# Optimization experiments

Measured on AMD Instinct MI355X. Metric: run time of the kernel, lower is better.

The kernel has to match this reference:

```python
import jax, jax.numpy as jnp
import numpy as np

# Model constants (solved parameter set; precip and water_efficiency from source)
TS = 0.0001
PRECIP = 1.845
WATER_EFFICIENCY = 0.449
SEEP_RATE = 0.2
UPTAKE_RATE = 1.0
ETA = 3.0
Q = 1.0
MORT_RATE = 0.3
D2 = 1.0
D3 = 0.05


def laplacian(x):
    # 3x3 5-point Laplacian stencil with replicate (edge) padding, x: [B,1,H,W]
    xp = jnp.pad(x, ((0, 0), (0, 0), (1, 1), (1, 1)), mode='edge')
    return (xp[:, :, :-2, 1:-1] + xp[:, :, 2:, 1:-1]
            + xp[:, :, 1:-1, :-2] + xp[:, :, 1:-1, 2:] - 4.0 * x)


def setup_inputs() -> dict:
    key = jax.random.key(0)
    k1, k2, k3 = jax.random.split(key, 3)
    shape = (16, 1, 1024, 1024)
    w = jax.random.uniform(k1, shape, dtype=jnp.float32)
    b = jax.random.uniform(k2, shape, dtype=jnp.float32)
    T = jax.random.uniform(k3, shape, dtype=jnp.float32)
    return {"w": w, "b": b, "T": T}


def reference(w, b, T):
    uptake = UPTAKE_RATE * w * b * (1.0 + ETA * b ** Q)
    dw = (D2 * laplacian(w) - SEEP_RATE * w + PRECIP - uptake) * TS
    db = (D3 * laplacian(b) - MORT_RATE * T * b + WATER_EFFICIENCY * uptake) * TS
    return (w + dw, b + db)
```

## Files before the change

### kernel.cpp

```cpp
#include <hip/hip_runtime.h>


namespace {
constexpr int IMGS = 16;
constexpr int H = 1024;
constexpr int W = 1024;
constexpr size_t PLANE = (size_t)H * W;
}

__global__ __launch_bounds__(256) void nca_step(
    const float* __restrict__ wg, const float* __restrict__ bg,
    const float* __restrict__ Tg, float* __restrict__ owg,
    float* __restrict__ obg)
{
    const int nwg = gridDim.x;
    const int cpx = nwg >> 3;
    const int bid = blockIdx.x;
    const int swz = (bid & 7) * cpx + (bid >> 3);

    const int img = swz >> 10;
    const int y   = swz & (H - 1);
    const int t   = threadIdx.x;
    const int x0  = t << 2;

    const float* wp = wg + (size_t)img * PLANE;
    const float* bp = bg + (size_t)img * PLANE;
    const float* Tp = Tg + (size_t)img * PLANE;

    const int yu = (y > 0)     ? (y - 1) : 0;
    const int yd = (y < H - 1) ? (y + 1) : (H - 1);

    const float* wrow = wp + (size_t)y * W;
    const float* brow = bp + (size_t)y * W;

    const float4 cw = *(const float4*)(wrow + x0);
    const float4 uw = *(const float4*)(wp + (size_t)yu * W + x0);
    const float4 dw = *(const float4*)(wp + (size_t)yd * W + x0);
    const float4 cb = *(const float4*)(brow + x0);
    const float4 ub = *(const float4*)(bp + (size_t)yu * W + x0);
    const float4 db = *(const float4*)(bp + (size_t)yd * W + x0);
    const float4 cT = *(const float4*)(Tp + (size_t)y * W + x0);

    const float wl = (x0 > 0)     ? wrow[x0 - 1] : cw.x;
    const float wr = (x0 + 4 < W) ? wrow[x0 + 4] : cw.w;
    const float bl = (x0 > 0)     ? brow[x0 - 1] : cb.x;
    const float br = (x0 + 4 < W) ? brow[x0 + 4] : cb.w;

    float lw[4], lb[4];
    lw[0] = uw.x + dw.x + wl   + cw.y - 4.0f * cw.x;
    lw[1] = uw.y + dw.y + cw.x + cw.z - 4.0f * cw.y;
    lw[2] = uw.z + dw.z + cw.y + cw.w - 4.0f * cw.z;
    lw[3] = uw.w + dw.w + cw.z + wr   - 4.0f * cw.w;

    lb[0] = ub.x + db.x + bl   + cb.y - 4.0f * cb.x;
    lb[1] = ub.y + db.y + cb.x + cb.z - 4.0f * cb.y;
    lb[2] = ub.z + db.z + cb.y + cb.w - 4.0f * cb.z;
    lb[3] = ub.w + db.w + cb.z + br   - 4.0f * cb.w;

    const float wv[4] = {cw.x, cw.y, cw.z, cw.w};
    const float bv[4] = {cb.x, cb.y, cb.z, cb.w};
    const float Tv[4] = {cT.x, cT.y, cT.z, cT.w};

    float4 ow4, ob4;
    float* owp = &ow4.x;
    float* obp = &ob4.x;
#pragma unroll
    for (int i = 0; i < 4; ++i) {
        const float up = wv[i] * bv[i] * (1.0f + 3.0f * bv[i]);
        owp[i] = wv[i] + (lw[i] - 0.2f * wv[i] + 1.845f - up) * 1e-4f;
        obp[i] = bv[i] + (0.05f * lb[i] - 0.3f * Tv[i] * bv[i] + 0.449f * up) * 1e-4f;
    }

    const size_t oidx = (size_t)img * PLANE + (size_t)y * W + x0;
    *(float4*)(owg + oidx) = ow4;
    *(float4*)(obg + oidx) = ob4;
}

extern "C" void kernel_launch(void* const* d_in, const int* in_sizes, int n_in,
                              void* d_out, int out_size, void* d_ws, size_t ws_size,
                              hipStream_t stream) {
    const float* w = (const float*)d_in[0];
    const float* b = (const float*)d_in[1];
    const float* T = (const float*)d_in[2];
    float* ow = (float*)d_out;
    float* ob = ow + (size_t)IMGS * PLANE;

    dim3 grid(IMGS * H);
    dim3 block(W / 4);
    nca_step<<<grid, block, 0, stream>>>(w, b, T, ow, ob);
}
```

Baseline: 280.3 us.

## Process four rows per block with register row reuse, shuffles, nontemporal IO

Each block now computes four consecutive rows and keeps six rows of w and b in registers, so vertical neighbours are reused instead of reloaded. Horizontal neighbours come from wave shuffles, and only the edge lanes fall back to scalar global loads. T loads and the output stores use nontemporal hints to reduce cache pollution. The grid shrinks by a factor of four, and each thread holds more registers and more loads in flight.

```diff
diff --git a/kernel.cpp b/kernel.cpp
--- a/kernel.cpp
+++ b/kernel.cpp
@@ -6,7 +6,10 @@
 constexpr int H = 1024;
 constexpr int W = 1024;
 constexpr size_t PLANE = (size_t)H * W;
+constexpr int RPB = 4;
 }
+
+typedef float f4 __attribute__((ext_vector_type(4)));
 
 __global__ __launch_bounds__(256) void nca_step(
     const float* __restrict__ wg, const float* __restrict__ bg,
@@ -18,62 +21,75 @@
     const int bid = blockIdx.x;
     const int swz = (bid & 7) * cpx + (bid >> 3);
 
-    const int img = swz >> 10;
-    const int y   = swz & (H - 1);
-    const int t   = threadIdx.x;
-    const int x0  = t << 2;
+    const int img = swz >> 8;
+    const int r0  = (swz & 255) * RPB;
+    const int t    = threadIdx.x;
+    const int lane = t & 63;
+    const int x0   = t << 2;
 
     const float* wp = wg + (size_t)img * PLANE;
     const float* bp = bg + (size_t)img * PLANE;
     const float* Tp = Tg + (size_t)img * PLANE;
 
-    const int yu = (y > 0)     ? (y - 1) : 0;
-    const int yd = (y < H - 1) ? (y + 1) : (H - 1);
+    const int rm1 = (r0 > 0)       ? r0 - 1   : 0;
+    const int rp4 = (r0 + RPB < H) ? r0 + RPB : H - 1;
 
-    const float* wrow = wp + (size_t)y * W;
-    const float* brow = bp + (size_t)y * W;
+    f4 wv[RPB + 2], bv[RPB + 2], Tv[RPB];
+    wv[0] = *(const f4*)(wp + (size_t)rm1 * W + x0);
+    bv[0] = *(const f4*)(bp + (size_t)rm1 * W + x0);
+#pragma unroll
+    for (int i = 0; i < RPB; ++i) {
+        wv[i + 1] = *(const f4*)(wp + (size_t)(r0 + i) * W + x0);
+        bv[i + 1] = *(const f4*)(bp + (size_t)(r0 + i) * W + x0);
+        Tv[i] = __builtin_nontemporal_load((const f4*)(Tp + (size_t)(r0 + i) * W + x0));
+    }
+    wv[RPB + 1] = *(const f4*)(wp + (size_t)rp4 * W + x0);
+    bv[RPB + 1] = *(const f4*)(bp + (size_t)rp4 * W + x0);
 
-    const float4 cw = *(const float4*)(wrow + x0);
-    const float4 uw = *(const float4*)(wp + (size_t)yu * W + x0);
-    const float4 dw = *(const float4*)(wp + (size_t)yd * W + x0);
-    const float4 cb = *(const float4*)(brow + x0);
-    const float4 ub = *(const float4*)(bp + (size_t)yu * W + x0);
-    const float4 db = *(const float4*)(bp + (size_t)yd * W + x0);
-    const float4 cT = *(const float4*)(Tp + (size_t)y * W + x0);
+#pragma unroll
+    for (int i = 0; i < RPB; ++i) {
+        const f4 cw = wv[i + 1], uw = wv[i], dw = wv[i + 2];
+        const f4 cb = bv[i + 1], ub = bv[i], db = bv[i + 2];
+        const f4 cT = Tv[i];
 
-    const float wl = (x0 > 0)     ? wrow[x0 - 1] : cw.x;
-    const float wr = (x0 + 4 < W) ? wrow[x0 + 4] : cw.w;
-    const float bl = (x0 > 0)     ? brow[x0 - 1] : cb.x;
-    const float br = (x0 + 4 < W) ? brow[x0 + 4] : cb.w;
+        float wl = __shfl_up(cw.w, 1);
+        float wr = __shfl_down(cw.x, 1);
+        float bl = __shfl_up(cb.w, 1);
+        float br = __shfl_down(cb.x, 1);
+        const float* wrow = wp + (size_t)(r0 + i) * W;
+        const float* brow = bp + (size_t)(r0 + i) * W;
+        if (lane == 0) {
+            wl = (x0 > 0) ? wrow[x0 - 1] : cw.x;
+            bl = (x0 > 0) ? brow[x0 - 1] : cb.x;
+        }
+        if (lane == 63) {
+            wr = (x0 + 4 < W) ? wrow[x0 + 4] : cw.w;
+            br = (x0 + 4 < W) ? brow[x0 + 4] : cb.w;
+        }
 
-    float lw[4], lb[4];
-    lw[0] = uw.x + dw.x + wl   + cw.y - 4.0f * cw.x;
-    lw[1] = uw.y + dw.y + cw.x + cw.z - 4.0f * cw.y;
-    lw[2] = uw.z + dw.z + cw.y + cw.w - 4.0f * cw.z;
-    lw[3] = uw.w + dw.w + cw.z + wr   - 4.0f * cw.w;
+        f4 lw, lb;
+        lw.x = uw.x + dw.x + wl   + cw.y - 4.0f * cw.x;
+        lw.y = uw.y + dw.y + cw.x + cw.z - 4.0f * cw.y;
+        lw.z = uw.z + dw.z + cw.y + cw.w - 4.0f * cw.z;
+        lw.w = uw.w + dw.w + cw.z + wr   - 4.0f * cw.w;
 
-    lb[0] = ub.x + db.x + bl   + cb.y - 4.0f * cb.x;
-    lb[1] = ub.y + db.y + cb.x + cb.z - 4.0f * cb.y;
-    lb[2] = ub.z + db.z + cb.y + cb.w - 4.0f * cb.z;
-    lb[3] = ub.w + db.w + cb.z + br   - 4.0f * cb.w;
+        lb.x = ub.x + db.x + bl   + cb.y - 4.0f * cb.x;
+        lb.y = ub.y + db.y + cb.x + cb.z - 4.0f * cb.y;
+        lb.z = ub.z + db.z + cb.y + cb.w - 4.0f * cb.z;
+        lb.w = ub.w + db.w + cb.z + br   - 4.0f * cb.w;
 
-    const float wv[4] = {cw.x, cw.y, cw.z, cw.w};
-    const float bv[4] = {cb.x, cb.y, cb.z, cb.w};
-    const float Tv[4] = {cT.x, cT.y, cT.z, cT.w};
+        f4 ow4, ob4;
+#pragma unroll
+        for (int j = 0; j < 4; ++j) {
+            const float up = cw[j] * cb[j] * (1.0f + 3.0f * cb[j]);
+            ow4[j] = cw[j] + (lw[j] - 0.2f * cw[j] + 1.845f - up) * 1e-4f;
+            ob4[j] = cb[j] + (0.05f * lb[j] - 0.3f * cT[j] * cb[j] + 0.449f * up) * 1e-4f;
+        }
 
-    float4 ow4, ob4;
-    float* owp = &ow4.x;
-    float* obp = &ob4.x;
-#pragma unroll
-    for (int i = 0; i < 4; ++i) {
-        const float up = wv[i] * bv[i] * (1.0f + 3.0f * bv[i]);
-        owp[i] = wv[i] + (lw[i] - 0.2f * wv[i] + 1.845f - up) * 1e-4f;
-        obp[i] = bv[i] + (0.05f * lb[i] - 0.3f * Tv[i] * bv[i] + 0.449f * up) * 1e-4f;
+        const size_t oidx = (size_t)img * PLANE + (size_t)(r0 + i) * W + x0;
+        __builtin_nontemporal_store(ow4, (f4*)(owg + oidx));
+        __builtin_nontemporal_store(ob4, (f4*)(obg + oidx));
     }
-
-    const size_t oidx = (size_t)img * PLANE + (size_t)y * W + x0;
-    *(float4*)(owg + oidx) = ow4;
-    *(float4*)(obg + oidx) = ob4;
 }
 
 extern "C" void kernel_launch(void* const* d_in, const int* in_sizes, int n_in,
@@ -85,7 +101,7 @@
     float* ow = (float*)d_out;
     float* ob = ow + (size_t)IMGS * PLANE;
 
-    dim3 grid(IMGS * H);
+    dim3 grid(IMGS * (H / RPB));
     dim3 block(W / 4);
     nca_step<<<grid, block, 0, stream>>>(w, b, T, ow, ob);
 }
```

Result: no change. 284.7 us (+1.6%).
